# Kernel optimization log

Measured on AMD Instinct MI355X. Metric: run time of the kernel, lower is better.

Reference implementation:

```python
import jax, jax.numpy as jnp
import numpy as np

# dims
B, N, D = 4, 1024, 768
H, HD = 12, 64            # num_heads, head_dim (routed q heads = top-H experts)
EA = 24                   # num_attn_experts
EF, KF = 8, 2             # num_ffd_experts, ffd_heads (top-k for FFN MoE)
HS = int(4 * D) // KF     # ffn expert head_size = 1536
T = 9                     # task_num
S = 1                     # shared FFN experts: max(1, int(8*0.1))


def layernorm(x, g, b, eps=1e-5):
    m = x.mean(-1, keepdims=True)
    v = ((x - m) ** 2).mean(-1, keepdims=True)
    return (x - m) * jax.lax.rsqrt(v + eps) * g + b


def setup_inputs() -> dict:
    key = jax.random.key(0)
    ks = jax.random.split(key, 16)
    s = 0.02
    rn = lambda k, shp: jax.random.normal(k, shp, dtype=jnp.float32)
    return {
        "x": rn(ks[0], (B, N, D)),
        "task_bh": 3,
        "ln1_g": jnp.ones((D,), jnp.float32), "ln1_b": jnp.zeros((D,), jnp.float32),
        "ln2_g": jnp.ones((D,), jnp.float32), "ln2_b": jnp.zeros((D,), jnp.float32),
        "gate_a": rn(ks[1], (T, D, EA)) * s,
        "Wq_in": rn(ks[2], (EA, D, HD)) * s,
        "Wq_out": rn(ks[3], (EA, HD, D)) * s,
        "W_kv": rn(ks[4], (D, 2 * HD)) * s, "b_kv": jnp.zeros((2 * HD,), jnp.float32),
        "gate_f": rn(ks[5], (T, D, EF)) * s,
        "W1f": rn(ks[6], (EF, D, HS)) * s, "b1f": jnp.zeros((EF, HS), jnp.float32),
        "W2f": rn(ks[7], (EF, HS, D)) * s, "b_out": jnp.zeros((D,), jnp.float32),
        "Ws1": rn(ks[8], (S, D, HS)) * s, "bs1": jnp.zeros((S, HS), jnp.float32),
        "Ws2": rn(ks[9], (S, HS, D)) * s,
    }


def _route(h, gate_w, k):
    # h: [B,N,D], gate_w: [D,E] -> normalized top-k weights + one-hot dispatch
    probs = jax.nn.softmax(jnp.einsum("bnd,de->bne", h, gate_w), axis=-1)
    topv, topi = jax.lax.top_k(probs, k)                 # [B,N,k]
    topv = topv / topv.sum(-1, keepdims=True)
    oh = jax.nn.one_hot(topi, probs.shape[-1], dtype=h.dtype)  # [B,N,k,E]
    return topv, oh


def reference(x, task_bh, ln1_g, ln1_b, ln2_g, ln2_b, gate_a, Wq_in, Wq_out,
              W_kv, b_kv, gate_f, W1f, b1f, W2f, b_out, Ws1, bs1, Ws2):
    # --- MoE attention (routed q heads, shared single-head k/v) ---
    h = layernorm(x, ln1_g, ln1_b)
    topv, oh = _route(h, gate_a[task_bh], H)             # [B,N,H], [B,N,H,EA]
    h_all = jnp.einsum("bnd,edh->bneh", h, Wq_in)        # all-expert q projections
    q = jnp.einsum("bnke,bneh->bnkh", oh, h_all)         # gathered q heads [B,N,H,HD]
    kv = h @ W_kv + b_kv
    kk, vv = kv[..., :HD], kv[..., HD:]                  # [B,N,HD]
    att = jnp.einsum("bihd,bjd->bhij", q, kk) * (HD ** -0.5)
    att = jax.nn.softmax(att, axis=-1)
    o = jnp.einsum("bhij,bjd->bihd", att, vv)            # [B,N,H,HD]
    dense = jnp.einsum("bnk,bnke,bnkh->bneh", topv, oh, o)  # scatter to experts
    y = jnp.einsum("bneh,ehd->bnd", dense, Wq_out)       # gated expert output proj
    x = x + y

    # --- MoE FFN (top-KF routed experts + shared experts) ---
    h = layernorm(x, ln2_g, ln2_b)
    topv, oh = _route(h, gate_f[task_bh], KF)            # [B,N,KF], [B,N,KF,EF]
    h_all = jax.nn.gelu(jnp.einsum("bnd,edh->bneh", h, W1f) + b1f, approximate=False)
    wdense = jnp.einsum("bnk,bnke->bne", topv, oh)       # per-expert gate weights
    y = jnp.einsum("bne,bneh,ehd->bnd", wdense, h_all, W2f) + b_out
    hs = jax.nn.gelu(jnp.einsum("bnd,sdh->bnsh", h, Ws1) + bs1, approximate=False)
    y = y + jnp.einsum("bnsh,shd->bnd", hs, Ws2)         # always-on shared experts
    return x + y
```

## Files before the change

### kernel.cpp

```cpp
#include <hip/hip_runtime.h>
#include <hip/hip_bf16.h>

#define NTOK 4096
#define DDIM 768
#define NEA  24
#define NHEAD 12
#define HDIM 64
#define NEF  8
#define HSD  1536
#define SEQL 1024
#define NB   4
#define MAXT64 200
#define NQKV 1664

using bf16 = __hip_bfloat16;

typedef float v4f __attribute__((ext_vector_type(4)));
typedef short v8s __attribute__((ext_vector_type(8)));
typedef __bf16 v8bf __attribute__((ext_vector_type(8)));

typedef __attribute__((address_space(3))) unsigned lds_u32_t;
typedef const __attribute__((address_space(1))) unsigned glb_u32_t;

__device__ __forceinline__ void gload16(const void* g, void* l) {
  __builtin_amdgcn_global_load_lds((glb_u32_t*)g, (lds_u32_t*)l, 16, 0, 0);
}

__device__ __forceinline__ float gelu_f(float x) {
  return 0.5f * x * (1.0f + erff(x * 0.70710678118654752440f));
}

__device__ __forceinline__ short f2bf_s(float x) {
  bf16 h = __float2bfloat16(x);
  return __builtin_bit_cast(short, h);
}

__device__ __forceinline__ int xcd_swz(int lin, int nwg) {
  return (lin & 7) * (nwg >> 3) + (lin >> 3);
}

__device__ __forceinline__ void gemm_core(const short* gA0, const short* gA1,
                                          const short* gB0, const short* gB1,
                                          short* lA, short* lB, int steps,
                                          v4f (&acc)[4][4])
{
  const int tid = threadIdx.x;
  const int w = tid >> 6, l = tid & 63;
  const int wr = (w >> 1) * 64, wc = (w & 1) * 64;
  const int fr = l & 15, ko = (l >> 4) * 8;
  const int sb = w * 1024;
  gload16(gA0, lA + sb); gload16(gA1, lA + sb + 512);
  gload16(gB0, lB + sb); gload16(gB1, lB + sb + 512);
  gA0 += 32; gA1 += 32; gB0 += 32; gB1 += 32;
  __syncthreads();
  int cur = 0;
  for (int s = 0; s < steps; ++s) {
    const int nxt = cur ^ 1;
    if (s + 1 < steps) {
      gload16(gA0, lA + nxt * 4096 + sb);
      gload16(gA1, lA + nxt * 4096 + sb + 512);
      gload16(gB0, lB + nxt * 4096 + sb);
      gload16(gB1, lB + nxt * 4096 + sb + 512);
      gA0 += 32; gA1 += 32; gB0 += 32; gB1 += 32;
    }
    const short* bA = lA + cur * 4096;
    const short* bB = lB + cur * 4096;
    v8s av[4], bv[4];
#pragma unroll
    for (int mi = 0; mi < 4; ++mi)
      av[mi] = *(const v8s*)(bA + (wr + mi * 16 + fr) * 32 + ko);
#pragma unroll
    for (int ni = 0; ni < 4; ++ni)
      bv[ni] = *(const v8s*)(bB + (wc + ni * 16 + fr) * 32 + ko);
#pragma unroll
    for (int mi = 0; mi < 4; ++mi)
#pragma unroll
      for (int ni = 0; ni < 4; ++ni)
        acc[mi][ni] = __builtin_amdgcn_mfma_f32_16x16x32_bf16(
            __builtin_bit_cast(v8bf, av[mi]), __builtin_bit_cast(v8bf, bv[ni]),
            acc[mi][ni], 0, 0, 0);
    __syncthreads();
    cur = nxt;
  }
}

template<int EPI>
__global__ __launch_bounds__(256, 4) void k_gemm(const short* __restrict__ A,
    const short* __restrict__ Bt, float* __restrict__ C,
    const float* __restrict__ addsrc, int N, int K)
{
  const int nwg = gridDim.x * gridDim.y;
  const int swz = xcd_swz(blockIdx.x + gridDim.x * blockIdx.y, nwg);
  const int m0 = (swz % gridDim.x) * 128, n0 = (swz / gridDim.x) * 128;
  __shared__ __align__(16) short lA[2 * 128 * 32];
  __shared__ __align__(16) short lB[2 * 128 * 32];
  const int tid = threadIdx.x, w = tid >> 6, l = tid & 63;
  const int ca = w * 128 + l, cb = ca + 64;
  const short* gA0 = A + (size_t)(m0 + (ca >> 2)) * K + (ca & 3) * 8;
  const short* gA1 = A + (size_t)(m0 + (cb >> 2)) * K + (cb & 3) * 8;
  const short* gB0 = Bt + (size_t)(n0 + (ca >> 2)) * K + (ca & 3) * 8;
  const short* gB1 = Bt + (size_t)(n0 + (cb >> 2)) * K + (cb & 3) * 8;
  v4f acc[4][4];
  v4f z = {0.f, 0.f, 0.f, 0.f};
#pragma unroll
  for (int i = 0; i < 4; ++i)
#pragma unroll
    for (int j = 0; j < 4; ++j) acc[i][j] = z;
  gemm_core(gA0, gA1, gB0, gB1, lA, lB, K >> 5, acc);
  const int wr = (w >> 1) * 64, wc = (w & 1) * 64;
  const int fr = l & 15, rq = (l >> 4) * 4;
#pragma unroll
  for (int mi = 0; mi < 4; ++mi)
#pragma unroll
    for (int ni = 0; ni < 4; ++ni)
#pragma unroll
      for (int j = 0; j < 4; ++j) {
        int rg = m0 + wr + mi * 16 + rq + j;
        int cg = n0 + wc + ni * 16 + fr;
        float v = acc[mi][ni][j];
        if (EPI == 2) v += addsrc[(size_t)rg * N + cg];
        C[(size_t)rg * N + cg] = v;
      }
}

template<int PHASE>
__global__ __launch_bounds__(64) void k_moe1w(
    const short* __restrict__ Aact, const short* __restrict__ Wt,
    const short* __restrict__ Wst, const float* __restrict__ b1f,
    const float* __restrict__ bs1, const float* __restrict__ wsl,
    const int* __restrict__ off, const int* __restrict__ cnt,
    const int* __restrict__ list, const int* __restrict__ tmeta,
    const int* __restrict__ ntl, short* __restrict__ outb,
    float* __restrict__ outf)
{
  constexpr int K = (PHASE == 0) ? DDIM : HSD;
  constexpr int N = (PHASE == 0) ? HSD : DDIM;
  const int nwg = gridDim.x * gridDim.y;
  const int swz = xcd_swz(blockIdx.x + gridDim.x * blockIdx.y, nwg);
  const int ti = swz % gridDim.x;
  const int n0 = (swz / gridDim.x) * 64;
  if (ti >= ntl[0]) return;
  const int mm = tmeta[ti];
  const int e = mm >> 20;
  const int r0 = mm & 0xFFFFF;
  const int base = (e < 8) ? off[e] : NTOK * 2;
  const int c    = (e < 8) ? cnt[e] : NTOK;
  const int rows = c - r0;
  const short* Bt = (e < 8) ? Wt + (size_t)e * N * K : Wst;
  __shared__ __align__(16) short lA[2 * 64 * 32];
  __shared__ __align__(16) short lB[2 * 64 * 32];
  const int l = threadIdx.x;

  auto arowptr = [&](int r) -> const short* {
    int re = (r < rows) ? r : (rows - 1);
    int slot = base + r0 + re;
    if (PHASE == 0) {
      int tok = (e < 8) ? list[slot] : (slot - NTOK * 2);
      return Aact + (size_t)tok * DDIM;
    }
    return Aact + (size_t)slot * HSD;
  };
  const short* gA[4];
  const short* gB[4];
#pragma unroll
  for (int i = 0; i < 4; ++i) {
    int ch = i * 64 + l;
    int r = ch >> 2, c8 = (ch & 3) * 8;
    gA[i] = arowptr(r) + c8;
    gB[i] = Bt + (size_t)(n0 + r) * K + c8;
  }
  v4f acc[4][4];
  v4f z = {0.f, 0.f, 0.f, 0.f};
#pragma unroll
  for (int i = 0; i < 4; ++i)
#pragma unroll
    for (int j = 0; j < 4; ++j) acc[i][j] = z;

  asm volatile("s_waitcnt vmcnt(0)" ::: "memory");

  auto stage = [&](int buf) {
    short* bA = lA + buf * 2048;
    short* bB = lB + buf * 2048;
#pragma unroll
    for (int i = 0; i < 4; ++i) { gload16(gA[i], bA + i * 512); gA[i] += 32; }
#pragma unroll
    for (int i = 0; i < 4; ++i) { gload16(gB[i], bB + i * 512); gB[i] += 32; }
  };
  const int steps = K >> 5;
  const int fr = l & 15, ko = (l >> 4) * 8;
  stage(0);
  int cur = 0;
  for (int s = 0; s < steps; ++s) {
    if (s + 1 < steps) {
      stage(cur ^ 1);
      asm volatile("s_waitcnt vmcnt(8)" ::: "memory");
    } else {
      asm volatile("s_waitcnt vmcnt(0)" ::: "memory");
    }
    __builtin_amdgcn_sched_barrier(0);
    const short* bA = lA + cur * 2048;
    const short* bB = lB + cur * 2048;
    v8s av[4], bv[4];
#pragma unroll
    for (int mi = 0; mi < 4; ++mi)
      av[mi] = *(const v8s*)(bA + (mi * 16 + fr) * 32 + ko);
#pragma unroll
    for (int ni = 0; ni < 4; ++ni)
      bv[ni] = *(const v8s*)(bB + (ni * 16 + fr) * 32 + ko);
#pragma unroll
    for (int mi = 0; mi < 4; ++mi)
#pragma unroll
      for (int ni = 0; ni < 4; ++ni)
        acc[mi][ni] = __builtin_amdgcn_mfma_f32_16x16x32_bf16(
            __builtin_bit_cast(v8bf, av[mi]), __builtin_bit_cast(v8bf, bv[ni]),
            acc[mi][ni], 0, 0, 0);
    cur ^= 1;
  }

  const int rq = (l >> 4) * 4;
  const float* bias = (PHASE == 0) ? ((e < 8) ? b1f + e * HSD : bs1) : nullptr;
#pragma unroll
  for (int mi = 0; mi < 4; ++mi)
#pragma unroll
    for (int ni = 0; ni < 4; ++ni)
#pragma unroll
      for (int j = 0; j < 4; ++j) {
        int rl = mi * 16 + rq + j;
        if (rl >= rows) continue;
        int slot = base + r0 + rl;
        int cg = n0 + ni * 16 + fr;
        float v = acc[mi][ni][j];
        if (PHASE == 0) {
          v = gelu_f(v + bias[cg]);
          outb[(size_t)slot * HSD + cg] = f2bf_s(v);
        } else {
          outf[(size_t)slot * DDIM + cg] = v * wsl[slot];
        }
      }
}

__global__ __launch_bounds__(256) void k_ln(const float* __restrict__ x,
    const float* __restrict__ g, const float* __restrict__ b,
    float* __restrict__ hf, bf16* __restrict__ hb)
{
  const size_t t = blockIdx.x;
  const float* xr = x + t * DDIM;
  int tid = threadIdx.x;
  float v0 = xr[tid], v1 = xr[tid + 256], v2 = xr[tid + 512];
  float s = v0 + v1 + v2;
  float q = v0 * v0 + v1 * v1 + v2 * v2;
  for (int m = 32; m >= 1; m >>= 1) { s += __shfl_xor(s, m); q += __shfl_xor(q, m); }
  __shared__ float rs[4], rq[4];
  int w = tid >> 6, l = tid & 63;
  if (l == 0) { rs[w] = s; rq[w] = q; }
  __syncthreads();
  s = rs[0] + rs[1] + rs[2] + rs[3];
  q = rq[0] + rq[1] + rq[2] + rq[3];
  float mean = s * (1.f / DDIM);
  float var = q * (1.f / DDIM) - mean * mean;
  float inv = rsqrtf(var + 1e-5f);
  float vv[3] = {v0, v1, v2};
#pragma unroll
  for (int i = 0; i < 3; ++i) {
    int d = tid + i * 256;
    float y = (vv[i] - mean) * inv * g[d] + b[d];
    hf[t * DDIM + d] = y;
    hb[t * DDIM + d] = __float2bfloat16(y);
  }
}

__global__ __launch_bounds__(256) void k_routeA(const float* __restrict__ hf,
    const float* __restrict__ gt, int* __restrict__ topi, float* __restrict__ topv)
{
  const int t = blockIdx.x * 4 + (threadIdx.x >> 6);
  const int l = threadIdx.x & 63;
  const float* h = hf + (size_t)t * DDIM;
  float hr[12];
#pragma unroll
  for (int m = 0; m < 12; ++m) hr[m] = h[l + 64 * m];
  float lg[NEA];
#pragma unroll
  for (int e = 0; e < NEA; ++e) {
    const float* ge = gt + e * DDIM;
    float a = 0.f;
#pragma unroll
    for (int m = 0; m < 12; ++m) a += hr[m] * ge[l + 64 * m];
#pragma unroll
    for (int m = 32; m >= 1; m >>= 1) a += __shfl_xor(a, m);
    lg[e] = a;
  }
  unsigned used = 0;
  int sel[NHEAD]; float bvk[NHEAD];
#pragma unroll
  for (int k = 0; k < NHEAD; ++k) {
    float bv = -3e30f; int best = 0;
#pragma unroll
    for (int e = 0; e < NEA; ++e)
      if (!((used >> e) & 1u) && lg[e] > bv) { bv = lg[e]; best = e; }
    used |= 1u << best; sel[k] = best; bvk[k] = bv;
  }
  const float mx = bvk[0];
  float pvk[NHEAD], ssum = 0.f;
#pragma unroll
  for (int k = 0; k < NHEAD; ++k) { pvk[k] = expf(bvk[k] - mx); ssum += pvk[k]; }
  const float inv = 1.f / ssum;
  if (l == 0) {
#pragma unroll
    for (int k = 0; k < NHEAD; ++k) {
      topi[t * NHEAD + k] = sel[k];
      topv[t * NHEAD + k] = pvk[k] * inv;
    }
  }
}

__global__ __launch_bounds__(256) void k_routeF(const float* __restrict__ hf,
    const float* __restrict__ gt, int* __restrict__ ef, float* __restrict__ wf,
    int* __restrict__ cnt)
{
  const int t = blockIdx.x * 4 + (threadIdx.x >> 6);
  const int l = threadIdx.x & 63;
  const float* h = hf + (size_t)t * DDIM;
  float hr[12];
#pragma unroll
  for (int m = 0; m < 12; ++m) hr[m] = h[l + 64 * m];
  float lg[NEF];
#pragma unroll
  for (int e = 0; e < NEF; ++e) {
    const float* ge = gt + e * DDIM;
    float a = 0.f;
#pragma unroll
    for (int m = 0; m < 12; ++m) a += hr[m] * ge[l + 64 * m];
#pragma unroll
    for (int m = 32; m >= 1; m >>= 1) a += __shfl_xor(a, m);
    lg[e] = a;
  }
  unsigned used = 0;
  int sel[2]; float bvk[2];
#pragma unroll
  for (int k = 0; k < 2; ++k) {
    float bv = -3e30f; int best = 0;
#pragma unroll
    for (int e = 0; e < NEF; ++e)
      if (!((used >> e) & 1u) && lg[e] > bv) { bv = lg[e]; best = e; }
    used |= 1u << best; sel[k] = best; bvk[k] = bv;
  }
  const float mx = bvk[0];
  float p0 = expf(bvk[0] - mx), p1 = expf(bvk[1] - mx);
  const float inv = 1.f / (p0 + p1);
  if (l == 0) {
    ef[t * 2 + 0] = sel[0]; wf[t * 2 + 0] = p0 * inv;
    ef[t * 2 + 1] = sel[1]; wf[t * 2 + 1] = p1 * inv;
    atomicAdd(&cnt[sel[0]], 1);
    atomicAdd(&cnt[sel[1]], 1);
  }
}

__global__ void k_packGT(const float* __restrict__ src, const int* __restrict__ task,
                         float* __restrict__ dst, int E)
{
  int idx = blockIdx.x * 256 + threadIdx.x;
  if (idx >= E * DDIM) return;
  int e = idx / DDIM, d = idx - e * DDIM;
  dst[idx] = src[(size_t)task[0] * DDIM * E + (size_t)d * E + e];
}

__global__ void k_off(const int* __restrict__ cnt, int* __restrict__ off,
                      int* __restrict__ cur, int* __restrict__ tmeta,
                      int* __restrict__ ntl)
{
  if (threadIdx.x == 0 && blockIdx.x == 0) {
    int a = 0;
    for (int e = 0; e < NEF; ++e) { off[e] = a; cur[e] = a; a += cnt[e]; }
    off[NEF] = a;
    int n = 0;
    for (int e = 0; e < NEF; ++e)
      for (int r = 0; r < cnt[e]; r += 64) tmeta[n++] = (e << 20) | r;
    for (int r = 0; r < NTOK; r += 64) tmeta[n++] = (8 << 20) | r;
    ntl[0] = n;
  }
}

__global__ void k_fill(const int* __restrict__ ef, const float* __restrict__ wf,
                       int* __restrict__ cur, int* __restrict__ list,
                       float* __restrict__ wsl, int* __restrict__ sof)
{
  int t = blockIdx.x * 256 + threadIdx.x;
  if (t >= NTOK) return;
  for (int k = 0; k < 2; ++k) {
    int e = ef[t * 2 + k];
    int slot = atomicAdd(&cur[e], 1);
    list[slot] = t;
    wsl[slot] = wf[t * 2 + k];
    sof[t * 2 + k] = slot;
  }
  list[NTOK * 2 + t] = t;
  wsl[NTOK * 2 + t] = 1.f;
}

__global__ void k_qgather(const float* __restrict__ hallq, const int* __restrict__ topi,
                          bf16* __restrict__ q)
{
  int idx = blockIdx.x * 256 + threadIdx.x;
  int t = idx / (NHEAD * HDIM);
  int rem = idx - t * (NHEAD * HDIM);
  int k = rem >> 6, hd = rem & 63;
  q[idx] = __float2bfloat16(
      hallq[(size_t)t * NQKV + topi[t * NHEAD + k] * HDIM + hd]);
}

__global__ void k_packKV(const float* __restrict__ hallq, const float* __restrict__ bkv,
                         bf16* __restrict__ kvb)
{
  int idx = blockIdx.x * 256 + threadIdx.x;
  int t = idx >> 7, j = idx & 127;
  kvb[idx] = __float2bfloat16(hallq[(size_t)t * NQKV + 1536 + j] + bkv[j]);
}

__global__ void k_scatter(const float* __restrict__ o, const int* __restrict__ topi,
                          const float* __restrict__ topv, bf16* __restrict__ dense)
{
  int idx = blockIdx.x * 256 + threadIdx.x;
  int t = idx / (NHEAD * HDIM);
  int rem = idx - t * (NHEAD * HDIM);
  int k = rem >> 6, hd = rem & 63;
  float v = topv[t * NHEAD + k] * o[idx];
  dense[(size_t)t * (NEA * HDIM) + topi[t * NHEAD + k] * HDIM + hd] = __float2bfloat16(v);
}

__global__ __launch_bounds__(256, 2) void k_attn_mfma(const bf16* __restrict__ q,
    const bf16* __restrict__ kv, float* __restrict__ o)
{
  __shared__ __align__(16) short Qs[64 * 64];
  __shared__ __align__(16) short Ks[64 * 64];
  __shared__ __align__(16) short Vs[64 * 64];
  __shared__ __align__(16) short Ps[64 * 64];
  const int i0 = blockIdx.x * 64;
  const int h = blockIdx.y;
  const int b = blockIdx.z;
  const int tid = threadIdx.x;
  const int w = tid >> 6, l = tid & 63;
  const int g = l >> 4, fq = l & 15;
  const short* qg = (const short*)q;
  const short* kvg = (const short*)kv;

  {
    int c0 = tid, c1 = tid + 256;
    int r0 = c0 >> 3, s0 = (c0 & 7) ^ (r0 & 7);
    int r1 = c1 >> 3, s1 = (c1 & 7) ^ (r1 & 7);
    gload16(qg + ((size_t)((b * SEQL + i0 + r0) * NHEAD + h)) * HDIM + s0 * 8,
            Qs + w * 512);
    gload16(qg + ((size_t)((b * SEQL + i0 + r1) * NHEAD + h)) * HDIM + s1 * 8,
            Qs + 2048 + w * 512);
  }

  float m_run[4], l_run[4];
  v4f oacc[4];
#pragma unroll
  for (int r = 0; r < 4; ++r) { m_run[r] = -1e30f; l_run[r] = 0.f; }
#pragma unroll
  for (int nd = 0; nd < 4; ++nd) oacc[nd] = (v4f){0.f, 0.f, 0.f, 0.f};

  const int vj = tid & 63;
  const int vd0 = (tid >> 6) * 16;

  for (int jt = 0; jt < 16; ++jt) {
    if (jt) __syncthreads();
    {
      int c0 = tid, c1 = tid + 256;
      int r0 = c0 >> 3, s0 = (c0 & 7) ^ (r0 & 7);
      int r1 = c1 >> 3, s1 = (c1 & 7) ^ (r1 & 7);
      gload16(kvg + ((size_t)(b * SEQL + jt * 64 + r0)) * 128 + s0 * 8,
              Ks + w * 512);
      gload16(kvg + ((size_t)(b * SEQL + jt * 64 + r1)) * 128 + s1 * 8,
              Ks + 2048 + w * 512);
    }
    {
      const short* gv = kvg + ((size_t)(b * SEQL + jt * 64 + vj)) * 128 + 64 + vd0;
      v8s a0 = *(const v8s*)gv;
      v8s a1 = *(const v8s*)(gv + 8);
#pragma unroll
      for (int k2 = 0; k2 < 8; ++k2) {
        int d = vd0 + k2;
        Vs[d * 64 + (((vj >> 3) ^ (d & 7)) << 3) + (vj & 7)] = a0[k2];
      }
#pragma unroll
      for (int k2 = 0; k2 < 8; ++k2) {
        int d = vd0 + 8 + k2;
        Vs[d * 64 + (((vj >> 3) ^ (d & 7)) << 3) + (vj & 7)] = a1[k2];
      }
    }
    __syncthreads();

    v8s aq[2];
#pragma unroll
    for (int kk = 0; kk < 2; ++kk)
      aq[kk] = *(const v8s*)&Qs[(16 * w + fq) * 64 + (((kk * 4 + g) ^ (fq & 7)) << 3)];
    v4f sacc[4];
#pragma unroll
    for (int n = 0; n < 4; ++n) {
      sacc[n] = (v4f){0.f, 0.f, 0.f, 0.f};
#pragma unroll
      for (int kk = 0; kk < 2; ++kk) {
        v8s bk = *(const v8s*)&Ks[(16 * n + fq) * 64 + (((kk * 4 + g) ^ (fq & 7)) << 3)];
        sacc[n] = __builtin_amdgcn_mfma_f32_16x16x32_bf16(
            __builtin_bit_cast(v8bf, aq[kk]), __builtin_bit_cast(v8bf, bk),
            sacc[n], 0, 0, 0);
      }
    }
#pragma unroll
    for (int n = 0; n < 4; ++n) sacc[n] *= 0.125f;

#pragma unroll
    for (int r = 0; r < 4; ++r) {
      float mt = fmaxf(fmaxf(sacc[0][r], sacc[1][r]), fmaxf(sacc[2][r], sacc[3][r]));
      mt = fmaxf(mt, __shfl_xor(mt, 1));
      mt = fmaxf(mt, __shfl_xor(mt, 2));
      mt = fmaxf(mt, __shfl_xor(mt, 4));
      mt = fmaxf(mt, __shfl_xor(mt, 8));
      float mnew = fmaxf(m_run[r], mt);
      float corr = __expf(m_run[r] - mnew);
      float pv[4], ps = 0.f;
#pragma unroll
      for (int n = 0; n < 4; ++n) { pv[n] = __expf(sacc[n][r] - mnew); ps += pv[n]; }
      ps += __shfl_xor(ps, 1);
      ps += __shfl_xor(ps, 2);
      ps += __shfl_xor(ps, 4);
      ps += __shfl_xor(ps, 8);
      l_run[r] = l_run[r] * corr + ps;
      m_run[r] = mnew;
#pragma unroll
      for (int nd = 0; nd < 4; ++nd) oacc[nd][r] *= corr;
      int qrow = 16 * w + 4 * g + r;
#pragma unroll
      for (int n = 0; n < 4; ++n)
        Ps[qrow * 64 + (((2 * n + (fq >> 3)) ^ (qrow & 7)) << 3) + (fq & 7)] =
            f2bf_s(pv[n]);
    }
    asm volatile("s_waitcnt lgkmcnt(0)" ::: "memory");
    __builtin_amdgcn_sched_barrier(0);

#pragma unroll
    for (int kk = 0; kk < 2; ++kk) {
      v8s pa = *(const v8s*)&Ps[(16 * w + fq) * 64 + (((kk * 4 + g) ^ (fq & 7)) << 3)];
#pragma unroll
      for (int nd = 0; nd < 4; ++nd) {
        v8s vb = *(const v8s*)&Vs[(16 * nd + fq) * 64 + (((kk * 4 + g) ^ (fq & 7)) << 3)];
        oacc[nd] = __builtin_amdgcn_mfma_f32_16x16x32_bf16(
            __builtin_bit_cast(v8bf, pa), __builtin_bit_cast(v8bf, vb),
            oacc[nd], 0, 0, 0);
      }
    }
  }

#pragma unroll
  for (int r = 0; r < 4; ++r) {
    float inv = 1.f / l_run[r];
    int qgl = i0 + 16 * w + 4 * g + r;
#pragma unroll
    for (int nd = 0; nd < 4; ++nd)
      o[(((size_t)b * SEQL + qgl) * NHEAD + h) * HDIM + 16 * nd + fq] =
          oacc[nd][r] * inv;
  }
}

__global__ __launch_bounds__(256) void k_packT(const float* __restrict__ src,
                                               bf16* __restrict__ dst, int K, int N)
{
  __shared__ float tile[32][33];
  const size_t zoff = (size_t)blockIdx.z * K * N;
  const int k0 = blockIdx.x * 32, n0 = blockIdx.y * 32;
  const int tx = threadIdx.x & 31, ty = threadIdx.x >> 5;
#pragma unroll
  for (int i = 0; i < 32; i += 8)
    tile[ty + i][tx] = src[zoff + (size_t)(k0 + ty + i) * N + n0 + tx];
  __syncthreads();
#pragma unroll
  for (int i = 0; i < 32; i += 8)
    dst[zoff + (size_t)(n0 + ty + i) * K + k0 + tx] =
        __float2bfloat16(tile[tx][ty + i]);
}

__global__ void k_final(const float* __restrict__ x2, const float* __restrict__ bout,
                        const float* __restrict__ yp, const int* __restrict__ sof,
                        float* __restrict__ out)
{
  int idx = blockIdx.x * 256 + threadIdx.x;
  int t = idx / DDIM, d = idx - t * DDIM;
  int s0 = sof[2 * t], s1 = sof[2 * t + 1];
  out[idx] = x2[idx] + bout[d] + yp[(size_t)s0 * DDIM + d] + yp[(size_t)s1 * DDIM + d] +
             yp[((size_t)(NTOK * 2) + t) * DDIM + d];
}

extern "C" void kernel_launch(void* const* d_in, const int* in_sizes, int n_in,
                              void* d_out, int out_size, void* d_ws, size_t ws_size,
                              hipStream_t stream) {
  const float* x      = (const float*)d_in[0];
  const int*   task   = (const int*)d_in[1];
  const float* ln1g   = (const float*)d_in[2];
  const float* ln1b   = (const float*)d_in[3];
  const float* ln2g   = (const float*)d_in[4];
  const float* ln2b   = (const float*)d_in[5];
  const float* gate_a = (const float*)d_in[6];
  const float* wq_in  = (const float*)d_in[7];
  const float* wq_out = (const float*)d_in[8];
  const float* w_kv   = (const float*)d_in[9];
  const float* b_kv   = (const float*)d_in[10];
  const float* gate_f = (const float*)d_in[11];
  const float* w1f    = (const float*)d_in[12];
  const float* b1f    = (const float*)d_in[13];
  const float* w2f    = (const float*)d_in[14];
  const float* b_out  = (const float*)d_in[15];
  const float* ws1    = (const float*)d_in[16];
  const float* bs1    = (const float*)d_in[17];
  const float* ws2    = (const float*)d_in[18];

  char* W = (char*)d_ws;
  size_t off_ = 0;
  auto alloc = [&](size_t b) { size_t o = off_; off_ += (b + 255) & ~(size_t)255; return o; };
  size_t o_h1f   = alloc(12582912);
  size_t o_h1b   = alloc(6291456);
  size_t o_hallq = alloc(27262976);
  size_t o_hmid  = o_h1f;
  size_t o_q     = alloc(12582912);
  size_t o_o     = alloc(12582912);
  size_t o_dense = alloc(12582912);
  size_t o_ypart = o_q;
  size_t o_kvb   = alloc(1048576);
  size_t o_x2    = alloc(12582912);
  size_t o_h2f   = alloc(12582912);
  size_t o_h2b   = alloc(6291456);
  size_t o_btq   = alloc(2555904);
  size_t o_wqot  = alloc(2359296);
  size_t o_w1t   = alloc(18874368);
  size_t o_w2t   = alloc(18874368);
  size_t o_ws1t  = alloc(2359296);
  size_t o_ws2t  = alloc(2359296);
  size_t o_topi  = alloc(196608);
  size_t o_topv  = alloc(196608);
  size_t o_ef    = alloc(32768);
  size_t o_wf    = alloc(32768);
  size_t o_cnt   = alloc(1024);
  size_t o_offs  = alloc(1024);
  size_t o_cur   = alloc(1024);
  size_t o_list  = alloc(49152);
  size_t o_wsl   = alloc(49152);
  size_t o_sof   = alloc(32768);
  size_t o_tmeta = alloc(1024);
  size_t o_ntl   = alloc(256);
  size_t o_gta   = alloc(73728);
  size_t o_gtf   = alloc(24576);
  if (ws_size < off_) return;

  float* h1f   = (float*)(W + o_h1f);
  bf16*  h1b   = (bf16*)(W + o_h1b);
  float* hallq = (float*)(W + o_hallq);
  bf16*  qbb   = (bf16*)(W + o_q);
  float* ob    = (float*)(W + o_o);
  bf16*  dense = (bf16*)(W + o_dense);
  bf16*  kvbb  = (bf16*)(W + o_kvb);
  float* x2b   = (float*)(W + o_x2);
  float* h2f   = (float*)(W + o_h2f);
  bf16*  h2b   = (bf16*)(W + o_h2b);
  short* hmid  = (short*)(W + o_hmid);
  float* ypart = (float*)(W + o_ypart);
  int*   topi  = (int*)(W + o_topi);
  float* topv  = (float*)(W + o_topv);
  int*   efp   = (int*)(W + o_ef);
  float* wfp   = (float*)(W + o_wf);
  int*   cntp  = (int*)(W + o_cnt);
  int*   offp  = (int*)(W + o_offs);
  int*   curp  = (int*)(W + o_cur);
  int*   listp = (int*)(W + o_list);
  float* wslp  = (float*)(W + o_wsl);
  int*   sofp  = (int*)(W + o_sof);
  int*   tmeta = (int*)(W + o_tmeta);
  int*   ntl   = (int*)(W + o_ntl);
  float* gta   = (float*)(W + o_gta);
  float* gtf   = (float*)(W + o_gtf);

  k_packT<<<dim3(24, 2, 24), 256, 0, stream>>>(wq_in, (bf16*)(W + o_btq), 768, 64);
  k_packT<<<dim3(24, 4, 1), 256, 0, stream>>>(w_kv, (bf16*)(W + o_btq) + 1536 * 768, 768, 128);
  k_packT<<<dim3(48, 24, 1), 256, 0, stream>>>(wq_out, (bf16*)(W + o_wqot), 1536, 768);
  k_packT<<<dim3(24, 48, 8), 256, 0, stream>>>(w1f, (bf16*)(W + o_w1t), 768, 1536);
  k_packT<<<dim3(48, 24, 8), 256, 0, stream>>>(w2f, (bf16*)(W + o_w2t), 1536, 768);
  k_packT<<<dim3(24, 48, 1), 256, 0, stream>>>(ws1, (bf16*)(W + o_ws1t), 768, 1536);
  k_packT<<<dim3(48, 24, 1), 256, 0, stream>>>(ws2, (bf16*)(W + o_ws2t), 1536, 768);
  k_packGT<<<dim3(72), 256, 0, stream>>>(gate_a, task, gta, NEA);
  k_packGT<<<dim3(24), 256, 0, stream>>>(gate_f, task, gtf, NEF);

  (void)hipMemsetAsync(W + o_dense, 0, 12582912, stream);
  (void)hipMemsetAsync(W + o_cnt, 0, 64, stream);

  k_ln<<<NTOK, 256, 0, stream>>>(x, ln1g, ln1b, h1f, h1b);
  k_routeA<<<NTOK / 4, 256, 0, stream>>>(h1f, gta, topi, topv);

  k_gemm<0><<<dim3(32, 13), 256, 0, stream>>>((const short*)h1b, (const short*)(W + o_btq),
                                              hallq, nullptr, NQKV, 768);

  k_qgather<<<dim3(12288), 256, 0, stream>>>(hallq, topi, qbb);
  k_packKV<<<dim3(2048), 256, 0, stream>>>(hallq, b_kv, kvbb);
  k_attn_mfma<<<dim3(16, NHEAD, NB), 256, 0, stream>>>(qbb, kvbb, ob);
  k_scatter<<<dim3(12288), 256, 0, stream>>>(ob, topi, topv, dense);

  k_gemm<2><<<dim3(32, 6), 256, 0, stream>>>((const short*)dense, (const short*)(W + o_wqot),
                                             x2b, x, 768, 1536);

  k_ln<<<NTOK, 256, 0, stream>>>(x2b, ln2g, ln2b, h2f, h2b);
  k_routeF<<<NTOK / 4, 256, 0, stream>>>(h2f, gtf, efp, wfp, cntp);
  k_off<<<1, 1, 0, stream>>>(cntp, offp, curp, tmeta, ntl);
  k_fill<<<16, 256, 0, stream>>>(efp, wfp, curp, listp, wslp, sofp);

  k_moe1w<0><<<dim3(MAXT64, 24), 64, 0, stream>>>((const short*)h2b,
      (const short*)(W + o_w1t), (const short*)(W + o_ws1t), b1f, bs1, nullptr,
      offp, cntp, listp, tmeta, ntl, hmid, nullptr);
  k_moe1w<1><<<dim3(MAXT64, 12), 64, 0, stream>>>((const short*)hmid,
      (const short*)(W + o_w2t), (const short*)(W + o_ws2t), nullptr, nullptr, wslp,
      offp, cntp, listp, tmeta, ntl, nullptr, ypart);

  k_final<<<dim3(12288), 256, 0, stream>>>(x2b, b_out, ypart, sofp, (float*)d_out);
}
```

Baseline: 627.0 us.

## Retile MoE FFN GEMMs to 256x256 eight-wave blocks with split-K second phase

Replaces the single-wave 64x64 MoE expert GEMM with a 512-thread kernel that computes 256x256 output tiles. It uses K=64 stages, an XOR-swizzled LDS layout and barrier-synchronised double buffering. The second projection is split into two K halves across blockIdx.z and accumulated with float atomics into a buffer that is now zeroed by an added memset. The goal is more operand reuse per byte loaded and fewer, better-utilised workgroups. The costs are more padded rows per expert tile, 128KB of LDS per block, and atomic and memset traffic.

```diff
diff --git a/kernel.cpp b/kernel.cpp
--- a/kernel.cpp
+++ b/kernel.cpp
@@ -10,7 +10,7 @@
 #define HSD  1536
 #define SEQL 1024
 #define NB   4
-#define MAXT64 200
+#define MAXT256 56
 #define NQKV 1664
 
 using bf16 = __hip_bfloat16;
@@ -124,7 +124,7 @@
 }
 
 template<int PHASE>
-__global__ __launch_bounds__(64) void k_moe1w(
+__global__ __launch_bounds__(512, 2) void k_moe256(
     const short* __restrict__ Aact, const short* __restrict__ Wt,
     const short* __restrict__ Wst, const float* __restrict__ b1f,
     const float* __restrict__ bs1, const float* __restrict__ wsl,
@@ -138,7 +138,7 @@
   const int nwg = gridDim.x * gridDim.y;
   const int swz = xcd_swz(blockIdx.x + gridDim.x * blockIdx.y, nwg);
   const int ti = swz % gridDim.x;
-  const int n0 = (swz / gridDim.x) * 64;
+  const int n0 = (swz / gridDim.x) * 256;
   if (ti >= ntl[0]) return;
   const int mm = tmeta[ti];
   const int e = mm >> 20;
@@ -147,9 +147,10 @@
   const int c    = (e < 8) ? cnt[e] : NTOK;
   const int rows = c - r0;
   const short* Bt = (e < 8) ? Wt + (size_t)e * N * K : Wst;
-  __shared__ __align__(16) short lA[2 * 64 * 32];
-  __shared__ __align__(16) short lB[2 * 64 * 32];
-  const int l = threadIdx.x;
+  const int kbase = (PHASE == 1) ? (int)blockIdx.z * 768 : 0;
+  __shared__ __align__(16) short lA[2 * 256 * 64];
+  __shared__ __align__(16) short lB[2 * 256 * 64];
+  const int tid = threadIdx.x, w = tid >> 6, l = tid & 63;
 
   auto arowptr = [&](int r) -> const short* {
     int re = (r < rows) ? r : (rows - 1);
@@ -164,77 +165,84 @@
   const short* gB[4];
 #pragma unroll
   for (int i = 0; i < 4; ++i) {
-    int ch = i * 64 + l;
-    int r = ch >> 2, c8 = (ch & 3) * 8;
-    gA[i] = arowptr(r) + c8;
-    gB[i] = Bt + (size_t)(n0 + r) * K + c8;
-  }
-  v4f acc[4][4];
+    int ch = i * 512 + tid;
+    int r = ch >> 3, s8 = (ch & 7) ^ (r & 7);
+    gA[i] = arowptr(r) + s8 * 8 + kbase;
+    gB[i] = Bt + (size_t)(n0 + r) * K + s8 * 8 + kbase;
+  }
+  auto stage = [&](int buf) {
+#pragma unroll
+    for (int i = 0; i < 4; ++i) {
+      gload16(gA[i], lA + buf * 16384 + i * 4096 + w * 512);
+      gload16(gB[i], lB + buf * 16384 + i * 4096 + w * 512);
+      gA[i] += 64; gB[i] += 64;
+    }
+  };
+  const int wm = w >> 2, wn = w & 3;
+  const int fr = l & 15, g = l >> 4;
+
+  v4f acc[8][4];
   v4f z = {0.f, 0.f, 0.f, 0.f};
 #pragma unroll
-  for (int i = 0; i < 4; ++i)
+  for (int i = 0; i < 8; ++i)
 #pragma unroll
     for (int j = 0; j < 4; ++j) acc[i][j] = z;
 
-  asm volatile("s_waitcnt vmcnt(0)" ::: "memory");
-
-  auto stage = [&](int buf) {
-    short* bA = lA + buf * 2048;
-    short* bB = lB + buf * 2048;
-#pragma unroll
-    for (int i = 0; i < 4; ++i) { gload16(gA[i], bA + i * 512); gA[i] += 32; }
-#pragma unroll
-    for (int i = 0; i < 4; ++i) { gload16(gB[i], bB + i * 512); gB[i] += 32; }
-  };
-  const int steps = K >> 5;
-  const int fr = l & 15, ko = (l >> 4) * 8;
+  const int steps = 768 >> 6;
   stage(0);
+  __syncthreads();
   int cur = 0;
   for (int s = 0; s < steps; ++s) {
-    if (s + 1 < steps) {
-      stage(cur ^ 1);
-      asm volatile("s_waitcnt vmcnt(8)" ::: "memory");
-    } else {
-      asm volatile("s_waitcnt vmcnt(0)" ::: "memory");
-    }
-    __builtin_amdgcn_sched_barrier(0);
-    const short* bA = lA + cur * 2048;
-    const short* bB = lB + cur * 2048;
-    v8s av[4], bv[4];
-#pragma unroll
-    for (int mi = 0; mi < 4; ++mi)
-      av[mi] = *(const v8s*)(bA + (mi * 16 + fr) * 32 + ko);
-#pragma unroll
-    for (int ni = 0; ni < 4; ++ni)
-      bv[ni] = *(const v8s*)(bB + (ni * 16 + fr) * 32 + ko);
-#pragma unroll
-    for (int mi = 0; mi < 4; ++mi)
-#pragma unroll
-      for (int ni = 0; ni < 4; ++ni)
-        acc[mi][ni] = __builtin_amdgcn_mfma_f32_16x16x32_bf16(
-            __builtin_bit_cast(v8bf, av[mi]), __builtin_bit_cast(v8bf, bv[ni]),
-            acc[mi][ni], 0, 0, 0);
-    cur ^= 1;
+    const int nxt = cur ^ 1;
+    if (s + 1 < steps) stage(nxt);
+    const short* bA = lA + cur * 16384;
+    const short* bB = lB + cur * 16384;
+    v8s av[8][2], bv[4][2];
+#pragma unroll
+    for (int mi = 0; mi < 8; ++mi) {
+      int r = wm * 128 + mi * 16 + fr;
+#pragma unroll
+      for (int kk = 0; kk < 2; ++kk)
+        av[mi][kk] = *(const v8s*)(bA + r * 64 + (((kk * 4 + g) ^ (fr & 7)) << 3));
+    }
+#pragma unroll
+    for (int ni = 0; ni < 4; ++ni) {
+      int r = wn * 64 + ni * 16 + fr;
+#pragma unroll
+      for (int kk = 0; kk < 2; ++kk)
+        bv[ni][kk] = *(const v8s*)(bB + r * 64 + (((kk * 4 + g) ^ (fr & 7)) << 3));
+    }
+#pragma unroll
+    for (int kk = 0; kk < 2; ++kk)
+#pragma unroll
+      for (int mi = 0; mi < 8; ++mi)
+#pragma unroll
+        for (int ni = 0; ni < 4; ++ni)
+          acc[mi][ni] = __builtin_amdgcn_mfma_f32_16x16x32_bf16(
+              __builtin_bit_cast(v8bf, av[mi][kk]),
+              __builtin_bit_cast(v8bf, bv[ni][kk]), acc[mi][ni], 0, 0, 0);
+    __syncthreads();
+    cur = nxt;
   }
 
   const int rq = (l >> 4) * 4;
   const float* bias = (PHASE == 0) ? ((e < 8) ? b1f + e * HSD : bs1) : nullptr;
 #pragma unroll
-  for (int mi = 0; mi < 4; ++mi)
+  for (int mi = 0; mi < 8; ++mi)
 #pragma unroll
     for (int ni = 0; ni < 4; ++ni)
 #pragma unroll
       for (int j = 0; j < 4; ++j) {
-        int rl = mi * 16 + rq + j;
+        int rl = wm * 128 + mi * 16 + rq + j;
         if (rl >= rows) continue;
         int slot = base + r0 + rl;
-        int cg = n0 + ni * 16 + fr;
+        int cg = n0 + wn * 64 + ni * 16 + fr;
         float v = acc[mi][ni][j];
         if (PHASE == 0) {
           v = gelu_f(v + bias[cg]);
           outb[(size_t)slot * HSD + cg] = f2bf_s(v);
         } else {
-          outf[(size_t)slot * DDIM + cg] = v * wsl[slot];
+          atomicAdd(&outf[(size_t)slot * DDIM + cg], v * wsl[slot]);
         }
       }
 }
@@ -374,8 +382,8 @@
     off[NEF] = a;
     int n = 0;
     for (int e = 0; e < NEF; ++e)
-      for (int r = 0; r < cnt[e]; r += 64) tmeta[n++] = (e << 20) | r;
-    for (int r = 0; r < NTOK; r += 64) tmeta[n++] = (8 << 20) | r;
+      for (int r = 0; r < cnt[e]; r += 256) tmeta[n++] = (e << 20) | r;
+    for (int r = 0; r < NTOK; r += 256) tmeta[n++] = (8 << 20) | r;
     ntl[0] = n;
   }
 }
@@ -705,15 +713,17 @@
   k_gemm<2><<<dim3(32, 6), 256, 0, stream>>>((const short*)dense, (const short*)(W + o_wqot),
                                              x2b, x, 768, 1536);
 
+  (void)hipMemsetAsync(W + o_ypart, 0, 37748736, stream);
+
   k_ln<<<NTOK, 256, 0, stream>>>(x2b, ln2g, ln2b, h2f, h2b);
   k_routeF<<<NTOK / 4, 256, 0, stream>>>(h2f, gtf, efp, wfp, cntp);
   k_off<<<1, 1, 0, stream>>>(cntp, offp, curp, tmeta, ntl);
   k_fill<<<16, 256, 0, stream>>>(efp, wfp, curp, listp, wslp, sofp);
 
-  k_moe1w<0><<<dim3(MAXT64, 24), 64, 0, stream>>>((const short*)h2b,
+  k_moe256<0><<<dim3(MAXT256, 6), 512, 0, stream>>>((const short*)h2b,
       (const short*)(W + o_w1t), (const short*)(W + o_ws1t), b1f, bs1, nullptr,
       offp, cntp, listp, tmeta, ntl, hmid, nullptr);
-  k_moe1w<1><<<dim3(MAXT64, 12), 64, 0, stream>>>((const short*)hmid,
+  k_moe256<1><<<dim3(MAXT256, 3, 2), 512, 0, stream>>>((const short*)hmid,
       (const short*)(W + o_w2t), (const short*)(W + o_ws2t), nullptr, nullptr, wslp,
       offp, cntp, listp, tmeta, ntl, nullptr, ypart);
 
```

Measured after the change: 701.5 us. 11.9% more time.
